# Performance work log

Hardware: AMD Instinct MI355X
Metric: run time of the kernel (lower is better)

## Reference

```python
import jax, jax.numpy as jnp
import numpy as np
from jax.scipy.special import logsumexp

B, L, M, D = 8192, 1024, 128, 2  # batch, hilbert.size, bond dim, local_size
MACHINE_POW = 2


def setup_inputs() -> dict:
    key = jax.random.key(0)
    k1, k2 = jax.random.split(key)
    # configurations in the zero-magnetization sector: each row is a permutation
    # of L//2 zeros and L//2 ones (constrained HomogeneousHilbert)
    base = jnp.tile(jnp.arange(D, dtype=jnp.int32), L // D)  # (L,)
    inputs = jax.vmap(lambda k: jax.random.permutation(k, base))(jax.random.split(k1, B))
    # variational parameters epsilon: (local_size, M, size); centered at 1 so the
    # length-L multiplicative cache chain stays in fp32 range
    epsilon = 1.0 + 0.02 * jax.random.normal(k2, (D, M, L), dtype=jnp.float32)
    return {"inputs": inputs, "epsilon": epsilon}


def _conditionals(inputs, epsilon):
    # inputs: (B, L) int in [0, D); epsilon: (D, M, L)
    Bn, Ln = inputs.shape
    Dn, Mn, _ = epsilon.shape
    half = Ln // 2

    def scan_fun(carry, index):
        cache, n_spins = carry                       # (B, D, M), (B, D)
        prev = inputs[:, (index - 1) % Ln]           # (B,) previous-site state
        params_i = epsilon[:, :, index]              # (D, M)
        # irregular gather: cache[b, prev[b], :]
        gathered = jnp.take_along_axis(cache, prev[:, None, None], axis=1)[:, 0, :]  # (B, M)
        prods = params_i[None, :, :] * gathered[:, None, :]  # (B, D, M)
        log_psi = jnp.sum(prods, axis=-1)            # (B, D) sum over bond dim
        n_spins = jnp.where(index > 0,
                            n_spins + jax.nn.one_hot(prev, Dn, dtype=jnp.int32),
                            n_spins)
        # zero-magnetization renormalization: -inf once a local state is exhausted
        renorm = jnp.log(jnp.heaviside((half - n_spins).astype(log_psi.dtype), 0.0))
        return (prods, n_spins), log_psi + renorm

    cache0 = jnp.ones((Bn, Dn, Mn), epsilon.dtype)
    n0 = jnp.zeros((Bn, Dn), jnp.int32)
    _, log_psi = jax.lax.scan(scan_fun, (cache0, n0), jnp.arange(Ln))
    return jnp.transpose(log_psi, (1, 0, 2))  # (B, L, D)


def reference(inputs, epsilon):
    lp = _conditionals(inputs, epsilon)  # (B, L, D)
    # normalize conditionals over local states (machine_pow = 2)
    lp = lp - (1.0 / MACHINE_POW) * logsumexp(MACHINE_POW * lp, axis=-1, keepdims=True)
    # pick the log-conditional of the actual configuration at each site
    sel = jnp.take_along_axis(lp, inputs[:, :, None], axis=2)[:, :, 0]  # (B, L)
    # n_symm = 1 (default apply_symmetries): symmetrized logsumexp is identity
    return jnp.sum(sel, axis=1)  # (B,) log_psi
```

## Files before the change

### kernel.cpp

```cpp
#include <hip/hip_runtime.h>
#include <hip/hip_fp16.h>

typedef unsigned long long u64;
typedef unsigned int uint32;
typedef short short8 __attribute__((ext_vector_type(8)));
typedef float f32x4 __attribute__((ext_vector_type(4)));
typedef _Float16 h2 __attribute__((ext_vector_type(2)));

#define B_N 8192
#define L_N 1024
#define M_N 128
#define C_N 16
#define CH_N 64
#define HALF_N 512

#define OFF_W16  0
#define OFF_R16  0x40000
#define OFF_BITS 0x80000
#define OFF_LR   0x180000
#define OFF_RQ   0x1C0000
#define OFF_T    0x21C0000

#define PACK_BLK (B_N * L_N / 256)
#define EPS_BLK  32
#define ZERO_BLK 32

__device__ __forceinline__ unsigned short f32_bf16(float f) {
    union { float f; unsigned u; } x; x.f = f;
    unsigned u = x.u + 0x7FFFu + ((x.u >> 16) & 1u);
    return (unsigned short)(u >> 16);
}

__device__ __forceinline__ float fdot2(h2 a, h2 b, float c) {
#if __has_builtin(__builtin_amdgcn_fdot2)
    return __builtin_amdgcn_fdot2(a, b, c, false);
#else
    return (float)a[0] * (float)b[0] + (float)a[1] * (float)b[1] + c;
#endif
}

union HU { uint32 u; __half2 hh; h2 v2; };

__global__ __launch_bounds__(256) void k_prep(const int* __restrict__ inp,
        const float* __restrict__ eps, u64* __restrict__ bits,
        _Float16* __restrict__ w16, _Float16* __restrict__ r16,
        unsigned short* __restrict__ lrT, float* __restrict__ out) {
    int bid = blockIdx.x;
    if (bid < PACK_BLK) {
        int g = bid * 256 + threadIdx.x;
        int v = inp[g];
        u64 m = __ballot(v != 0);
        if ((threadIdx.x & 63) == 0) bits[g >> 6] = m;
        return;
    }
    bid -= PACK_BLK;
    if (bid < EPS_BLK) {
        int wid = threadIdx.x >> 6, lane = threadIdx.x & 63;
        int m = bid * 4 + wid;
        const float* e0 = eps + (size_t)m * L_N + lane * 16;
        const float* e1 = eps + (size_t)(M_N + m) * L_N + lane * 16;
        float a[16], b[16];
        #pragma unroll
        for (int j = 0; j < 16; j += 4) {
            *(float4*)&a[j] = *(const float4*)&e0[j];
            *(float4*)&b[j] = *(const float4*)&e1[j];
        }
        float local = 1.f;
        #pragma unroll
        for (int j = 0; j < 16; ++j) local *= a[j];
        float sc = local;
        #pragma unroll
        for (int d = 1; d < 64; d <<= 1) {
            float up = __shfl_up(sc, d);
            if (lane >= d) sc *= up;
        }
        float prev = __shfl_up(sc, 1);
        float E = (lane == 0) ? 1.f : prev;
        int i0 = lane * 16;
        #pragma unroll
        for (int j = 0; j < 16; ++j) {
            float rat = b[j] / a[j];
            w16[(size_t)(i0 + j) * M_N + m] = (_Float16)(E * (a[j] - b[j]));
            r16[(size_t)(i0 + j) * M_N + m] = (_Float16)rat;
            lrT[(size_t)m * L_N + i0 + j] = f32_bf16(__log2f(rat));
            E *= a[j];
        }
        return;
    }
    bid -= EPS_BLK;
    if (bid < ZERO_BLK) {
        out[bid * 256 + threadIdx.x] = 0.f;
    }
}

__global__ __launch_bounds__(256) void k_slog2(const u64* __restrict__ bits,
        const unsigned short* __restrict__ lrT, _Float16* __restrict__ Rq,
        int* __restrict__ T) {
    if (blockIdx.x >= 1024) {
        int b = (blockIdx.x - 1024) * 256 + threadIdx.x;
        const u64* brow = bits + (size_t)b * 16;
        int n1 = 0, n0 = 0, Tv = 1024;
        for (int wd = 0; wd < 16; ++wd) {
            u64 x = brow[wd];
            int pc = __popcll(x);
            if (n1 + pc < HALF_N && n0 + (64 - pc) < HALF_N) {
                n1 += pc; n0 += 64 - pc;
                continue;
            }
            int found = 0;
            for (int k = 0; k < 64; ++k) {
                if (n1 >= HALF_N || n0 >= HALF_N) { Tv = wd * 64 + k; found = 1; break; }
                int sb = (int)((x >> k) & 1);
                n1 += sb; n0 += 1 - sb;
            }
            if (!found) Tv = (wd + 1) * 64;
            break;
        }
        T[b] = Tv;
        return;
    }
    int btile = blockIdx.x >> 1;
    int half = blockIdx.x & 1;
    int wid = threadIdx.x >> 6, lane = threadIdx.x & 63;
    int col = lane & 15, quad = lane >> 4;
    int m = (half * 4 + wid) * 16 + col;
    int b_row = btile * 16 + col;
    const u64* brow = bits + (size_t)b_row * 16;
    const unsigned short* lrow = lrT + (size_t)m * L_N;

    f32x4 cum = (f32x4){0.f, 0.f, 0.f, 0.f};

    for (int c = 0; c < C_N; ++c) {
        #pragma unroll
        for (int reg = 0; reg < 4; ++reg) {
            int b = btile * 16 + quad * 4 + reg;
            Rq[((size_t)c * B_N + b) * M_N + m] = (_Float16)exp2f(cum[reg]);
        }
        u64 wv = brow[c];
        short8 a0, a1;
        #pragma unroll
        for (int j = 0; j < 8; ++j) {
            a0[j] = (short)((((wv >> (quad * 8 + j)) & 1) != 0) ? 0x3F80 : 0);
            a1[j] = (short)((((wv >> (32 + quad * 8 + j)) & 1) != 0) ? 0x3F80 : 0);
        }
        const unsigned short* bp = lrow + c * 64 + quad * 8;
        union { uint4 u; short8 s; } bf0, bf1;
        bf0.u = *(const uint4*)bp;
        bf1.u = *(const uint4*)(bp + 32);
        cum = __builtin_amdgcn_mfma_f32_16x16x32_bf16(a0, bf0.s, cum, 0, 0, 0);
        cum = __builtin_amdgcn_mfma_f32_16x16x32_bf16(a1, bf1.s, cum, 0, 0, 0);
    }
}

__global__ __launch_bounds__(256, 2) void k_main(const u64* __restrict__ bits,
        const _Float16* __restrict__ w16, const _Float16* __restrict__ r16,
        const _Float16* __restrict__ Rq, const int* __restrict__ T,
        float* __restrict__ out) {
    __shared__ _Float16 wbuf[CH_N * M_N];
    __shared__ _Float16 rbuf[CH_N * M_N];
    int c = blockIdx.x & (C_N - 1);
    int bblk = blockIdx.x >> 4;
    int lane = threadIdx.x & 63, wid = threadIdx.x >> 6;
    int s = lane & 7, g = lane >> 3;
    int b0 = bblk * 128 + wid * 32 + g * 4;
    int b_own = b0 + (s & 3);

    {
        const uint4* sw = (const uint4*)(w16 + (size_t)c * CH_N * M_N);
        const uint4* sr = (const uint4*)(r16 + (size_t)c * CH_N * M_N);
        uint4* dw = (uint4*)wbuf; uint4* dr = (uint4*)rbuf;
        #pragma unroll
        for (int t = 0; t < 4; ++t) {
            dw[threadIdx.x + t * 256] = sw[threadIdx.x + t * 256];
            dr[threadIdx.x + t * 256] = sr[threadIdx.x + t * 256];
        }
    }

    HU R2[4][8];
    #pragma unroll
    for (int nb = 0; nb < 4; ++nb) {
        union { uint4 q[2]; uint32 w[8]; } P;
        const uint4* src = (const uint4*)(Rq + ((size_t)c * B_N + (b0 + nb)) * M_N + s * 16);
        P.q[0] = src[0]; P.q[1] = src[1];
        #pragma unroll
        for (int j = 0; j < 8; ++j) R2[nb][j].u = P.w[j];
    }
    int Tb = T[b_own];
    u64 wb[4];
    #pragma unroll
    for (int nb = 0; nb < 4; ++nb) wb[nb] = bits[(size_t)(b0 + nb) * 16 + c];

    __syncthreads();

    const uint32 ONE2 = 0x3C003C00u;
    const float LOG2E2 = 2.885390082f;
    const float NHL2 = -0.3465735903f;
    float sum = 0.f;
    #pragma unroll
    for (int h = 0; h < 2; ++h) {
        uint32 wh[4];
        #pragma unroll
        for (int nb = 0; nb < 4; ++nb) wh[nb] = (uint32)(wb[nb] >> (h * 32));
        uint32 owa = (s & 1) ? wh[1] : wh[0];
        uint32 owb = (s & 1) ? wh[3] : wh[2];
        uint32 ow = (s & 2) ? owb : owa;

        int rel = Tb - (c * CH_N + h * 32);
        uint32 vmask = (rel <= 0) ? 0u : ((rel >= 32) ? 0xFFFFFFFFu : ((1u << rel) - 1u));

        for (int tt = 0; tt < 32; ++tt) {
            int base = (h * 32 + tt) * M_N + s * 16;
            union { uint4 q[2]; uint32 w[8]; h2 v2[8]; } W;
            union { uint4 q[2]; uint32 w[8]; } Rr;
            W.q[0] = *(const uint4*)&wbuf[base];
            W.q[1] = *((const uint4*)&wbuf[base] + 1);
            Rr.q[0] = *(const uint4*)&rbuf[base];
            Rr.q[1] = *((const uint4*)&rbuf[base] + 1);

            float d[4];
            #pragma unroll
            for (int nb = 0; nb < 4; ++nb) {
                float acc = 0.f;
                #pragma unroll
                for (int j = 0; j < 8; ++j) acc = fdot2(R2[nb][j].v2, W.v2[j], acc);
                d[nb] = acc;
            }
            float xa = (s & 1) ? d[1] : d[0];
            float ya = (s & 1) ? d[0] : d[1];
            xa += __shfl_xor(ya, 1);
            float xb = (s & 1) ? d[3] : d[2];
            float yb = (s & 1) ? d[2] : d[3];
            xb += __shfl_xor(yb, 1);
            float u2 = (s & 2) ? xb : xa;
            float v2 = (s & 2) ? xa : xb;
            u2 += __shfl_xor(v2, 2);
            u2 += __shfl_xor(u2, 4);
            float Dv = u2;

            int sbit = (ow >> tt) & 1;
            float y = sbit ? Dv : -Dv;
            float contr = NHL2 * __log2f(1.f + exp2f(LOG2E2 * y));
            sum += ((vmask >> tt) & 1) ? contr : 0.f;

            #pragma unroll
            for (int nb = 0; nb < 4; ++nb) {
                bool bit = (wh[nb] >> tt) & 1;
                #pragma unroll
                for (int j = 0; j < 8; ++j) {
                    HU sel; sel.u = bit ? Rr.w[j] : ONE2;
                    R2[nb][j].hh = __hmul2(R2[nb][j].hh, sel.hh);
                }
            }
        }
    }
    if (s < 4) atomicAdd(&out[b_own], sum);
}

extern "C" void kernel_launch(void* const* d_in, const int* in_sizes, int n_in,
                              void* d_out, int out_size, void* d_ws, size_t ws_size,
                              hipStream_t stream) {
    const int*   inputs  = (const int*)d_in[0];
    const float* epsilon = (const float*)d_in[1];
    float* out = (float*)d_out;

    char* ws = (char*)d_ws;
    _Float16* w16 = (_Float16*)(ws + OFF_W16);
    _Float16* r16 = (_Float16*)(ws + OFF_R16);
    u64*   bits   = (u64*)  (ws + OFF_BITS);
    unsigned short* lrT = (unsigned short*)(ws + OFF_LR);
    _Float16* Rq  = (_Float16*)(ws + OFF_RQ);
    int*   T      = (int*)  (ws + OFF_T);

    k_prep<<<PACK_BLK + EPS_BLK + ZERO_BLK, 256, 0, stream>>>(
        inputs, epsilon, bits, w16, r16, lrT, out);
    k_slog2<<<1024 + 32, 256, 0, stream>>>(bits, lrT, Rq, T);
    k_main<<<(B_N / 128) * C_N, 256, 0, stream>>>(bits, w16, r16, Rq, T, out);
}
```

Before: 181.6 us.

## Fuse prefix-log scan and threshold computation into main kernel

Removes the separate k_slog2 kernel. Each k_main block now computes its own chunk-start cache ratios with a bf16 MFMA over all preceding chunks, exponentiates them into shared memory and redistributes them to registers. The exhausted-site threshold is also computed inline per thread. This drops one launch and the global Rq/T round trip. In exchange, the prefix work is recomputed redundantly: chunk c repeats c chunks of MFMA, which gives triangular load imbalance across blocks and raises register pressure from the 64 accumulators.

```diff
diff --git a/kernel.cpp b/kernel.cpp
--- a/kernel.cpp
+++ b/kernel.cpp
@@ -13,13 +13,12 @@
 #define C_N 16
 #define CH_N 64
 #define HALF_N 512
+#define RSS 136
 
 #define OFF_W16  0
 #define OFF_R16  0x40000
 #define OFF_BITS 0x80000
 #define OFF_LR   0x180000
-#define OFF_RQ   0x1C0000
-#define OFF_T    0x21C0000
 
 #define PACK_BLK (B_N * L_N / 256)
 #define EPS_BLK  32
@@ -93,15 +92,28 @@
     }
 }
 
-__global__ __launch_bounds__(256) void k_slog2(const u64* __restrict__ bits,
-        const unsigned short* __restrict__ lrT, _Float16* __restrict__ Rq,
-        int* __restrict__ T) {
-    if (blockIdx.x >= 1024) {
-        int b = (blockIdx.x - 1024) * 256 + threadIdx.x;
-        const u64* brow = bits + (size_t)b * 16;
+__global__ __launch_bounds__(256, 2) void k_main(const u64* __restrict__ bits,
+        const _Float16* __restrict__ w16, const _Float16* __restrict__ r16,
+        const unsigned short* __restrict__ lrT, float* __restrict__ out) {
+    __shared__ __align__(16) char smem[128 * RSS * 2];
+    _Float16* RS = (_Float16*)smem;
+    _Float16* wbuf = (_Float16*)smem;
+    _Float16* rbuf = (_Float16*)(smem + 16384);
+
+    int c = blockIdx.x & (C_N - 1);
+    int bblk = blockIdx.x >> 4;
+    int lane = threadIdx.x & 63, wid = threadIdx.x >> 6;
+    int col = lane & 15, quad = lane >> 4;
+
+    int s = lane & 7, g = lane >> 3;
+    int b0 = bblk * 128 + wid * 32 + g * 4;
+    int b_own = b0 + (s & 3);
+    int Tb;
+    {
+        const u64* br = bits + (size_t)b_own * 16;
         int n1 = 0, n0 = 0, Tv = 1024;
         for (int wd = 0; wd < 16; ++wd) {
-            u64 x = brow[wd];
+            u64 x = br[wd];
             int pc = __popcll(x);
             if (n1 + pc < HALF_N && n0 + (64 - pc) < HALF_N) {
                 n1 += pc; n0 += 64 - pc;
@@ -116,54 +128,71 @@
             if (!found) Tv = (wd + 1) * 64;
             break;
         }
-        T[b] = Tv;
-        return;
-    }
-    int btile = blockIdx.x >> 1;
-    int half = blockIdx.x & 1;
-    int wid = threadIdx.x >> 6, lane = threadIdx.x & 63;
-    int col = lane & 15, quad = lane >> 4;
-    int m = (half * 4 + wid) * 16 + col;
-    int b_row = btile * 16 + col;
-    const u64* brow = bits + (size_t)b_row * 16;
-    const unsigned short* lrow = lrT + (size_t)m * L_N;
-
-    f32x4 cum = (f32x4){0.f, 0.f, 0.f, 0.f};
-
-    for (int c = 0; c < C_N; ++c) {
-        #pragma unroll
-        for (int reg = 0; reg < 4; ++reg) {
-            int b = btile * 16 + quad * 4 + reg;
-            Rq[((size_t)c * B_N + b) * M_N + m] = (_Float16)exp2f(cum[reg]);
-        }
-        u64 wv = brow[c];
-        short8 a0, a1;
-        #pragma unroll
-        for (int j = 0; j < 8; ++j) {
-            a0[j] = (short)((((wv >> (quad * 8 + j)) & 1) != 0) ? 0x3F80 : 0);
-            a1[j] = (short)((((wv >> (32 + quad * 8 + j)) & 1) != 0) ? 0x3F80 : 0);
-        }
-        const unsigned short* bp = lrow + c * 64 + quad * 8;
-        union { uint4 u; short8 s; } bf0, bf1;
-        bf0.u = *(const uint4*)bp;
-        bf1.u = *(const uint4*)(bp + 32);
-        cum = __builtin_amdgcn_mfma_f32_16x16x32_bf16(a0, bf0.s, cum, 0, 0, 0);
-        cum = __builtin_amdgcn_mfma_f32_16x16x32_bf16(a1, bf1.s, cum, 0, 0, 0);
-    }
-}
-
-__global__ __launch_bounds__(256, 2) void k_main(const u64* __restrict__ bits,
-        const _Float16* __restrict__ w16, const _Float16* __restrict__ r16,
-        const _Float16* __restrict__ Rq, const int* __restrict__ T,
-        float* __restrict__ out) {
-    __shared__ _Float16 wbuf[CH_N * M_N];
-    __shared__ _Float16 rbuf[CH_N * M_N];
-    int c = blockIdx.x & (C_N - 1);
-    int bblk = blockIdx.x >> 4;
-    int lane = threadIdx.x & 63, wid = threadIdx.x >> 6;
-    int s = lane & 7, g = lane >> 3;
-    int b0 = bblk * 128 + wid * 32 + g * 4;
-    int b_own = b0 + (s & 3);
+        Tb = Tv;
+    }
+
+    HU R2[4][8];
+    if (c > 0) {
+        f32x4 acc[2][8];
+        #pragma unroll
+        for (int bt = 0; bt < 2; ++bt)
+            #pragma unroll
+            for (int mt = 0; mt < 8; ++mt) acc[bt][mt] = (f32x4){0.f, 0.f, 0.f, 0.f};
+
+        int bg0 = bblk * 128 + (wid * 2 + 0) * 16 + col;
+        int bg1 = bblk * 128 + (wid * 2 + 1) * 16 + col;
+        for (int cp = 0; cp < c; ++cp) {
+            u64 wv0 = bits[(size_t)bg0 * 16 + cp];
+            u64 wv1 = bits[(size_t)bg1 * 16 + cp];
+            short8 a00, a01, a10, a11;
+            #pragma unroll
+            for (int j = 0; j < 8; ++j) {
+                a00[j] = (short)((((wv0 >> (quad * 8 + j)) & 1) != 0) ? 0x3F80 : 0);
+                a01[j] = (short)((((wv0 >> (32 + quad * 8 + j)) & 1) != 0) ? 0x3F80 : 0);
+                a10[j] = (short)((((wv1 >> (quad * 8 + j)) & 1) != 0) ? 0x3F80 : 0);
+                a11[j] = (short)((((wv1 >> (32 + quad * 8 + j)) & 1) != 0) ? 0x3F80 : 0);
+            }
+            #pragma unroll
+            for (int mt = 0; mt < 8; ++mt) {
+                int m = mt * 16 + col;
+                const unsigned short* bp = lrT + (size_t)m * L_N + cp * 64 + quad * 8;
+                union { uint4 u; short8 s; } bf0, bf1;
+                bf0.u = *(const uint4*)bp;
+                bf1.u = *(const uint4*)(bp + 32);
+                acc[0][mt] = __builtin_amdgcn_mfma_f32_16x16x32_bf16(a00, bf0.s, acc[0][mt], 0, 0, 0);
+                acc[0][mt] = __builtin_amdgcn_mfma_f32_16x16x32_bf16(a01, bf1.s, acc[0][mt], 0, 0, 0);
+                acc[1][mt] = __builtin_amdgcn_mfma_f32_16x16x32_bf16(a10, bf0.s, acc[1][mt], 0, 0, 0);
+                acc[1][mt] = __builtin_amdgcn_mfma_f32_16x16x32_bf16(a11, bf1.s, acc[1][mt], 0, 0, 0);
+            }
+        }
+        #pragma unroll
+        for (int bt = 0; bt < 2; ++bt) {
+            #pragma unroll
+            for (int mt = 0; mt < 8; ++mt) {
+                #pragma unroll
+                for (int reg = 0; reg < 4; ++reg) {
+                    int lb = (wid * 2 + bt) * 16 + quad * 4 + reg;
+                    RS[lb * RSS + mt * 16 + col] = (_Float16)exp2f(acc[bt][mt][reg]);
+                }
+            }
+        }
+        __syncthreads();
+        #pragma unroll
+        for (int nb = 0; nb < 4; ++nb) {
+            int lb = wid * 32 + g * 4 + nb;
+            const uint4* src = (const uint4*)&RS[lb * RSS + s * 16];
+            union { uint4 q[2]; uint32 w[8]; } P;
+            P.q[0] = src[0]; P.q[1] = src[1];
+            #pragma unroll
+            for (int j = 0; j < 8; ++j) R2[nb][j].u = P.w[j];
+        }
+        __syncthreads();
+    } else {
+        #pragma unroll
+        for (int nb = 0; nb < 4; ++nb)
+            #pragma unroll
+            for (int j = 0; j < 8; ++j) R2[nb][j].u = 0x3C003C00u;
+    }
 
     {
         const uint4* sw = (const uint4*)(w16 + (size_t)c * CH_N * M_N);
@@ -175,17 +204,6 @@
             dr[threadIdx.x + t * 256] = sr[threadIdx.x + t * 256];
         }
     }
-
-    HU R2[4][8];
-    #pragma unroll
-    for (int nb = 0; nb < 4; ++nb) {
-        union { uint4 q[2]; uint32 w[8]; } P;
-        const uint4* src = (const uint4*)(Rq + ((size_t)c * B_N + (b0 + nb)) * M_N + s * 16);
-        P.q[0] = src[0]; P.q[1] = src[1];
-        #pragma unroll
-        for (int j = 0; j < 8; ++j) R2[nb][j].u = P.w[j];
-    }
-    int Tb = T[b_own];
     u64 wb[4];
     #pragma unroll
     for (int nb = 0; nb < 4; ++nb) wb[nb] = bits[(size_t)(b0 + nb) * 16 + c];
@@ -268,11 +286,8 @@
     _Float16* r16 = (_Float16*)(ws + OFF_R16);
     u64*   bits   = (u64*)  (ws + OFF_BITS);
     unsigned short* lrT = (unsigned short*)(ws + OFF_LR);
-    _Float16* Rq  = (_Float16*)(ws + OFF_RQ);
-    int*   T      = (int*)  (ws + OFF_T);
 
     k_prep<<<PACK_BLK + EPS_BLK + ZERO_BLK, 256, 0, stream>>>(
         inputs, epsilon, bits, w16, r16, lrT, out);
-    k_slog2<<<1024 + 32, 256, 0, stream>>>(bits, lrT, Rq, T);
-    k_main<<<(B_N / 128) * C_N, 256, 0, stream>>>(bits, w16, r16, Rq, T, out);
-}
+    k_main<<<(B_N / 128) * C_N, 256, 0, stream>>>(bits, w16, r16, lrT, out);
+}
```

Measured after the change: 263.1 us. 44.9% more time.
